# Kernel optimization log

Measured on AMD Instinct MI355X. Metric: run time of the kernel, lower is better.

## Reference

```python
import jax, jax.numpy as jnp
import numpy as np

B, S, D, H = 2, 2048, 1024, 16
DH = D // H  # head dim = 64


def _split_heads(x):
    # [B,S,D] -> [B,H,S,DH]
    return x.reshape(B, S, H, DH).transpose(0, 2, 1, 3)


def setup_inputs() -> dict:
    key = jax.random.key(0)
    ks = jax.random.split(key, 14)
    sc = 1.0 / np.sqrt(D)
    p = {"hidden_states": jax.random.normal(ks[0], (B, S, D), jnp.float32)}
    names = ["Wq", "Wk1", "Wk2", "Wv1", "Wv2", "Wd"]
    for i, n in enumerate(names):
        p[n] = jax.random.normal(ks[1 + 2 * i], (D, D), jnp.float32) * sc
        p["b" + n[1:]] = jax.random.normal(ks[2 + 2 * i], (D,), jnp.float32) * 0.02
    return p


def reference(hidden_states, Wq, bq, Wk1, bk1, Wk2, bk2, Wv1, bv1, Wv2, bv2, Wd, bd):
    q = _split_heads(hidden_states @ Wq + bq)
    k1 = _split_heads(hidden_states @ Wk1 + bk1)
    k2 = _split_heads(hidden_states @ Wk2 + bk2)
    v1 = _split_heads(hidden_states @ Wv1 + bv1)
    v2 = _split_heads(hidden_states @ Wv2 + bv2)

    scores = jnp.einsum("bhqd,bhkd->bhqk", q, k1) / np.sqrt(DH)
    causal = jnp.tril(jnp.ones((S, S), dtype=bool))  # True = keep
    scores = jnp.where(causal, scores, -jnp.inf)
    probs = jax.nn.softmax(scores, axis=-1)

    ctx = jnp.einsum("bhqk,bhkd->bhqd", probs, v1)          # [B,H,S,DH]
    ctx = jnp.einsum("bhqd,bhkd->bhqk", ctx, k2)            # [B,H,S,S]
    ctx = jnp.einsum("bhqk,bhkd->bhqd", ctx, v2)            # [B,H,S,DH]

    ctx = ctx.transpose(0, 2, 1, 3).reshape(B, S, D)
    return ctx @ Wd + bd
```

## Files before the change

### kernel.cpp

```cpp
#include <hip/hip_runtime.h>
#include <hip/hip_bf16.h>

typedef __bf16 bf16x8 __attribute__((ext_vector_type(8)));
typedef float f32x4 __attribute__((ext_vector_type(4)));
using bf16 = __hip_bfloat16;

#define SEQ 2048
#define DM 1024
#define NH 16
#define DH 64
#define NBH 32
#define MR 4096

#define WAITBAR(N) asm volatile("s_waitcnt vmcnt(" #N ")\n\ts_barrier" ::: "memory")

static __device__ __forceinline__ void async_cp16(const void* gsrc, void* ldsdst) {
  __builtin_amdgcn_global_load_lds((__attribute__((address_space(1))) void*)gsrc,
                                   (__attribute__((address_space(3))) void*)ldsdst, 16, 0, 0);
}

static __device__ __forceinline__ unsigned short f2bfu(float f) {
  bf16 h = __float2bfloat16(f);
  unsigned short u; __builtin_memcpy(&u, &h, 2); return u;
}
static __device__ __forceinline__ unsigned int pack_bf2(float lo, float hi) {
  return (unsigned int)f2bfu(lo) | ((unsigned int)f2bfu(hi) << 16);
}

__global__ __launch_bounds__(256) void cast_x(const float* __restrict__ X, bf16* __restrict__ Xb) {
  long g = ((long)blockIdx.x * 256 + threadIdx.x) * 8;
  float4 a = *(const float4*)(X + g);
  float4 b = *(const float4*)(X + g + 4);
  unsigned short u[8];
  u[0]=f2bfu(a.x); u[1]=f2bfu(a.y); u[2]=f2bfu(a.z); u[3]=f2bfu(a.w);
  u[4]=f2bfu(b.x); u[5]=f2bfu(b.y); u[6]=f2bfu(b.z); u[7]=f2bfu(b.w);
  uint4 o; __builtin_memcpy(&o, u, 16);
  *(uint4*)(Xb + g) = o;
}

struct WPtrs { const float* w[6]; };

__global__ __launch_bounds__(256) void transpose_cast_w(WPtrs wp, bf16* __restrict__ WtAll) {
  const int z = blockIdx.z;
  const float* W = wp.w[z];
  bf16* Wt = WtAll + (long)z * DM * DM;
  __shared__ float Ts[32][33];
  int n0 = blockIdx.x * 32, k0 = blockIdx.y * 32;
  int tx = threadIdx.x, ty = threadIdx.y;
#pragma unroll
  for (int it = 0; it < 4; ++it)
    Ts[ty + 8*it][tx] = W[(long)(k0 + ty + 8*it) * DM + n0 + tx];
  __syncthreads();
#pragma unroll
  for (int it = 0; it < 4; ++it)
    Wt[(long)(n0 + ty + 8*it) * DM + k0 + tx] = __float2bfloat16(Ts[tx][ty + 8*it]);
}

struct ProjArgs {
  const float* bias[5];
  bf16* out[5];
};

__global__ __launch_bounds__(256, 2) void gemm_proj(const bf16* __restrict__ A,
                                                    const bf16* __restrict__ WtAll, ProjArgs p) {
  __shared__ alignas(16) bf16 SM[36864];
  bf16* As = SM;
  bf16* Bs = SM + 12288;
  const int tid = threadIdx.x;
  const int bid = blockIdx.x;
  const int wave = tid >> 6, lane = tid & 63, l15 = lane & 15, l4 = lane >> 4;
  const int wm = wave >> 1, wn = wave & 1;
  const int slot8 = (l4 ^ ((l15 >> 1) & 3)) * 8;
  const int prow = tid >> 2;
  const int cc = (tid & 3) ^ ((prow >> 1) & 3);
  char* dA = (char*)As + wave * 1024;
  char* dB = (char*)Bs + wave * 1024;

  if (bid < 512) {
    const int mt = bid & 31, nt = bid >> 5;
    const int m0 = mt * 128;
    const int z = nt >> 2;
    const int n0z = (nt & 3) * 256;
    const bf16* Bt = WtAll + (long)z * DM * DM + (long)n0z * DM;

    const bf16* sA0 = A  + (long)(m0 + prow) * DM + cc * 8;
    const bf16* sA1 = sA0 + 64L * DM;
    const bf16* sB0 = Bt + (long)prow * DM + cc * 8;
    const bf16* sB1 = sB0 + 64L * DM;
    const bf16* sB2 = sB0 + 128L * DM;
    const bf16* sB3 = sB0 + 192L * DM;

#define PSTAGE(KT_, BUF_) do {                                  \
    int ko_ = (KT_) * 32;                                       \
    async_cp16(sA0 + ko_, dA + (BUF_) * 8192);                  \
    async_cp16(sA1 + ko_, dA + (BUF_) * 8192 + 4096);           \
    async_cp16(sB0 + ko_, dB + (BUF_) * 16384);                 \
    async_cp16(sB1 + ko_, dB + (BUF_) * 16384 + 4096);          \
    async_cp16(sB2 + ko_, dB + (BUF_) * 16384 + 8192);          \
    async_cp16(sB3 + ko_, dB + (BUF_) * 16384 + 12288);         \
  } while (0)

    const int arow = wm * 64 + l15;
    const int brow = wn * 128 + l15;
    f32x4 acc[4][8] = {};

#define PCOMPUTE(BUF_) do {                                                        \
    const bf16* ab_ = As + (BUF_) * 4096;                                          \
    const bf16* bb_ = Bs + (BUF_) * 8192;                                          \
    bf16x8 af_[4], bq_[8];                                                         \
    _Pragma("unroll")                                                              \
    for (int i = 0; i < 4; ++i) af_[i] = *(const bf16x8*)(ab_ + (arow + i * 16) * 32 + slot8); \
    _Pragma("unroll")                                                              \
    for (int j = 0; j < 8; ++j) bq_[j] = *(const bf16x8*)(bb_ + (brow + j * 16) * 32 + slot8); \
    _Pragma("unroll")                                                              \
    for (int i = 0; i < 4; ++i)                                                    \
      _Pragma("unroll")                                                            \
      for (int j = 0; j < 8; ++j)                                                  \
        acc[i][j] = __builtin_amdgcn_mfma_f32_16x16x32_bf16(af_[i], bq_[j], acc[i][j], 0, 0, 0); \
  } while (0)

    PSTAGE(0, 0);
    PSTAGE(1, 1);
    int buf = 0;
#pragma unroll 1
    for (int k = 0; k < 31; ++k) {
      WAITBAR(6);
      if (k < 30) {
        int nb = buf + 2; if (nb > 2) nb -= 3;
        PSTAGE(k + 2, nb);
      }
      PCOMPUTE(buf);
      ++buf; if (buf > 2) buf = 0;
    }
    WAITBAR(0);
    PCOMPUTE(buf);
#undef PSTAGE
#undef PCOMPUTE

    const float* bias = p.bias[z];
    bf16* out = p.out[z];
    float bv[8];
#pragma unroll
    for (int j = 0; j < 8; ++j) bv[j] = bias[n0z + wn * 128 + j * 16 + l15];

    if (z < 2) {
      const float scale = (z == 0) ? 0.125f * 1.44269504f : 1.0f;
#pragma unroll
      for (int i = 0; i < 4; ++i)
#pragma unroll
        for (int j = 0; j < 8; ++j)
#pragma unroll
          for (int r = 0; r < 4; ++r) {
            int m = m0 + wm * 64 + i * 16 + l4 * 4 + r;
            int n = n0z + wn * 128 + j * 16 + l15;
            int b = m >> 11, s = m & 2047, hh = n >> 6, d = n & 63;
            out[((long)((b * NH + hh) * SEQ + s)) * DH + d] =
                __float2bfloat16((acc[i][j][r] + bv[j]) * scale);
          }
    } else {
      __syncthreads();
      bf16* Os = SM;
#pragma unroll
      for (int i = 0; i < 4; ++i)
#pragma unroll
        for (int j = 0; j < 8; ++j)
#pragma unroll
          for (int r = 0; r < 4; ++r) {
            int nl = wn * 128 + j * 16 + l15;
            int ml = wm * 64 + i * 16 + l4 * 4 + r;
            Os[nl * 136 + ml] = __float2bfloat16(acc[i][j][r] + bv[j]);
          }
      __syncthreads();
      {
        int nl = tid;
        int ng = n0z + nl;
        int hh = ng >> 6, d = ng & 63;
        int b = m0 >> 11, s0 = m0 & 2047;
        bf16* op = out + ((long)((b * NH + hh) * DH + d)) * SEQ + s0;
#pragma unroll
        for (int u = 0; u < 16; ++u)
          *(bf16x8*)(op + u * 8) = *(const bf16x8*)(Os + nl * 136 + u * 8);
      }
    }
  } else {
    const int tb = bid - 512;
    const int mt = tb & 31, nt16 = tb >> 5;
    const int m0 = mt * 128, n0 = nt16 * 64;
    const bf16* Bt = WtAll + 4L * DM * DM + (long)n0 * DM;

    const bf16* sA0 = A + (long)(m0 + prow) * DM + cc * 8;
    const bf16* sA1 = sA0 + 64L * DM;
    const bf16* sB0 = Bt + (long)prow * DM + cc * 8;

#define TSTAGE(KT_, BUF_) do {                                  \
    int ko_ = (KT_) * 32;                                       \
    async_cp16(sA0 + ko_, dA + (BUF_) * 8192);                  \
    async_cp16(sA1 + ko_, dA + (BUF_) * 8192 + 4096);           \
    async_cp16(sB0 + ko_, dB + (BUF_) * 4096);                  \
  } while (0)

    const int arow = wm * 64 + l15;
    const int brow = wn * 32 + l15;
    f32x4 acc2[4][2] = {};

#define TCOMPUTE(BUF_) do {                                                        \
    const bf16* ab_ = As + (BUF_) * 4096;                                          \
    const bf16* bb_ = Bs + (BUF_) * 2048;                                          \
    bf16x8 af_[4], bq_[2];                                                         \
    _Pragma("unroll")                                                              \
    for (int i = 0; i < 4; ++i) af_[i] = *(const bf16x8*)(ab_ + (arow + i * 16) * 32 + slot8); \
    _Pragma("unroll")                                                              \
    for (int j = 0; j < 2; ++j) bq_[j] = *(const bf16x8*)(bb_ + (brow + j * 16) * 32 + slot8); \
    _Pragma("unroll")                                                              \
    for (int i = 0; i < 4; ++i)                                                    \
      _Pragma("unroll")                                                            \
      for (int j = 0; j < 2; ++j)                                                  \
        acc2[i][j] = __builtin_amdgcn_mfma_f32_16x16x32_bf16(af_[i], bq_[j], acc2[i][j], 0, 0, 0); \
  } while (0)

    TSTAGE(0, 0);
    TSTAGE(1, 1);
    int buf = 0;
#pragma unroll 1
    for (int k = 0; k < 31; ++k) {
      WAITBAR(3);
      if (k < 30) {
        int nb = buf + 2; if (nb > 2) nb -= 3;
        TSTAGE(k + 2, nb);
      }
      TCOMPUTE(buf);
      ++buf; if (buf > 2) buf = 0;
    }
    WAITBAR(0);
    TCOMPUTE(buf);
#undef TSTAGE
#undef TCOMPUTE

    float bv2[2];
#pragma unroll
    for (int j = 0; j < 2; ++j) bv2[j] = p.bias[4][n0 + wn * 32 + j * 16 + l15];
    __syncthreads();
    bf16* Os = SM;
#pragma unroll
    for (int i = 0; i < 4; ++i)
#pragma unroll
      for (int j = 0; j < 2; ++j)
#pragma unroll
        for (int r = 0; r < 4; ++r) {
          int nl = wn * 32 + j * 16 + l15;
          int ml = wm * 64 + i * 16 + l4 * 4 + r;
          Os[nl * 136 + ml] = __float2bfloat16(acc2[i][j][r] + bv2[j]);
        }
    __syncthreads();
    {
      int nl = tid & 63, seg = tid >> 6;
      int ng = n0 + nl;
      int hh = ng >> 6, d = ng & 63;
      int b = m0 >> 11, s0 = m0 & 2047;
      bf16* op = p.out[4] + ((long)((b * NH + hh) * DH + d)) * SEQ + s0 + seg * 32;
#pragma unroll
      for (int u = 0; u < 4; ++u)
        *(bf16x8*)(op + u * 8) = *(const bf16x8*)(Os + nl * 136 + seg * 32 + u * 8);
    }
  }
}

__global__ __launch_bounds__(256, 3) void gemm_out(const bf16* __restrict__ A, const bf16* __restrict__ Bt,
                                                   const float* __restrict__ bias, float* __restrict__ out) {
  __shared__ alignas(16) bf16 As[3 * 128 * 32];
  __shared__ alignas(16) bf16 Bs[3 * 64 * 32];
  const int tid = threadIdx.x;
  const int bid = blockIdx.x;
  const int nt = bid & 15, mt = bid >> 4;
  const int m0 = mt * 128, n0 = nt * 64;
  const int wave = tid >> 6, lane = tid & 63, l15 = lane & 15, l4 = lane >> 4;
  const int wm = wave >> 1, wn = wave & 1;
  const int slot8 = (l4 ^ ((l15 >> 1) & 3)) * 8;
  const int prow = tid >> 2;
  const int cc = (tid & 3) ^ ((prow >> 1) & 3);
  const bf16* sA0 = A + (long)(m0 + prow) * DM + cc * 8;
  const bf16* sA1 = sA0 + 64L * DM;
  const bf16* sB0 = Bt + (long)(n0 + prow) * DM + cc * 8;
  char* dA = (char*)As + wave * 1024;
  char* dB = (char*)Bs + wave * 1024;

#define OSTAGE(KT_, BUF_) do {                                  \
    int ko_ = (KT_) * 32;                                       \
    async_cp16(sA0 + ko_, dA + (BUF_) * 8192);                  \
    async_cp16(sA1 + ko_, dA + (BUF_) * 8192 + 4096);           \
    async_cp16(sB0 + ko_, dB + (BUF_) * 4096);                  \
  } while (0)

  const int arow = wm * 64 + l15;
  const int brow = wn * 32 + l15;
  f32x4 acc2[4][2] = {};

#define OCOMPUTE(BUF_) do {                                                        \
    const bf16* ab_ = As + (BUF_) * 4096;                                          \
    const bf16* bb_ = Bs + (BUF_) * 2048;                                          \
    bf16x8 af_[4], bq_[2];                                                         \
    _Pragma("unroll")                                                              \
    for (int i = 0; i < 4; ++i) af_[i] = *(const bf16x8*)(ab_ + (arow + i * 16) * 32 + slot8); \
    _Pragma("unroll")                                                              \
    for (int j = 0; j < 2; ++j) bq_[j] = *(const bf16x8*)(bb_ + (brow + j * 16) * 32 + slot8); \
    _Pragma("unroll")                                                              \
    for (int i = 0; i < 4; ++i)                                                    \
      _Pragma("unroll")                                                            \
      for (int j = 0; j < 2; ++j)                                                  \
        acc2[i][j] = __builtin_amdgcn_mfma_f32_16x16x32_bf16(af_[i], bq_[j], acc2[i][j], 0, 0, 0); \
  } while (0)

  OSTAGE(0, 0);
  OSTAGE(1, 1);
  int buf = 0;
#pragma unroll 1
  for (int k = 0; k < 31; ++k) {
    WAITBAR(3);
    if (k < 30) {
      int nb = buf + 2; if (nb > 2) nb -= 3;
      OSTAGE(k + 2, nb);
    }
    OCOMPUTE(buf);
    ++buf; if (buf > 2) buf = 0;
  }
  WAITBAR(0);
  OCOMPUTE(buf);
#undef OSTAGE
#undef OCOMPUTE

  float bv[2];
#pragma unroll
  for (int j = 0; j < 2; ++j) bv[j] = bias[n0 + wn * 32 + j * 16 + l15];
#pragma unroll
  for (int i = 0; i < 4; ++i)
#pragma unroll
    for (int j = 0; j < 2; ++j)
#pragma unroll
      for (int r = 0; r < 4; ++r) {
        int m = m0 + wm * 64 + i * 16 + l4 * 4 + r;
        int n = n0 + wn * 32 + j * 16 + l15;
        out[(long)m * DM + n] = acc2[i][j][r] + bv[j];
      }
}

__global__ __launch_bounds__(256) void m_kernel(
    const bf16* __restrict__ k2t, const bf16* __restrict__ v2t, float* __restrict__ Mbuf)
{
  const int scx = blockIdx.x;
  const int bh = blockIdx.y;
  const int tid = threadIdx.x, wave = tid >> 6, lane = tid & 63, l15 = lane & 15, l4 = lane >> 4;
  const bf16* kp = k2t + (long)bh * DH * SEQ;
  const bf16* vp = v2t + (long)bh * DH * SEQ;
  __shared__ alignas(16) bf16 K2s[64 * 32];
  __shared__ alignas(16) bf16 V2s[64 * 32];
  f32x4 acc[4] = {};
  const int s0 = scx * 256;
  for (int kk = 0; kk < 256; kk += 32) {
    __syncthreads();
    {
      int c = tid, r = c >> 2, pp = c & 3;
      async_cp16(kp + (long)r * SEQ + s0 + kk + pp * 8, K2s + wave * 64 * 8);
      async_cp16(vp + (long)r * SEQ + s0 + kk + pp * 8, V2s + wave * 64 * 8);
    }
    __syncthreads();
    int arow = 16 * wave + l15;
    bf16x8 a = *(const bf16x8*)(K2s + arow * 32 + l4 * 8);
#pragma unroll
    for (int nb = 0; nb < 4; ++nb) {
      int col = nb * 16 + l15;
      bf16x8 b = *(const bf16x8*)(V2s + col * 32 + l4 * 8);
      acc[nb] = __builtin_amdgcn_mfma_f32_16x16x32_bf16(a, b, acc[nb], 0, 0, 0);
    }
  }
  float* Mp = Mbuf + (long)bh * 4096;
#pragma unroll
  for (int nb = 0; nb < 4; ++nb)
#pragma unroll
    for (int r = 0; r < 4; ++r) {
      int row = 16 * wave + l4 * 4 + r;
      int col = nb * 16 + l15;
      atomicAdd(Mp + row * 64 + col, acc[nb][r]);
    }
}

static __device__ __forceinline__ void redist(const unsigned int (&pk)[4][2], bf16x8 (&pb)[2],
                                              int l4, int l15) {
#pragma unroll
  for (int h = 0; h < 2; ++h) {
    unsigned int w4[4];
#pragma unroll
    for (int w = 0; w < 4; ++w) {
      int src = l15 + 16 * (2 * (l4 & 1) + (w >> 1));
      unsigned int va = (unsigned int)__shfl((int)pk[2 * h][w & 1], src);
      unsigned int vb = (unsigned int)__shfl((int)pk[2 * h + 1][w & 1], src);
      w4[w] = (l4 & 2) ? vb : va;
    }
    __builtin_memcpy(&pb[h], w4, 16);
  }
}

__global__ __launch_bounds__(256) void attn_fused(
    const bf16* __restrict__ q,
    const bf16* __restrict__ k1,
    const bf16* __restrict__ v1t,
    const float* __restrict__ Mbuf,
    bf16* __restrict__ ctx2)
{
  const int bid = blockIdx.x;
  const int xcd = bid & 7, ii = bid >> 3;
  const int bh = (xcd << 2) | (ii & 3);
  const int qpair = ii >> 2;
  const int bb = bh >> 4, hh = bh & 15;
  const int tid = threadIdx.x, wave = tid >> 6, lane = tid & 63;
  const int l15 = lane & 15, l4 = lane >> 4;
  const bf16* qp = q   + (long)bh * SEQ * DH;
  const bf16* kp = k1  + (long)bh * SEQ * DH;
  const bf16* vp = v1t + (long)bh * DH * SEQ;
  const float* Mp = Mbuf + (long)bh * 4096;

  __shared__ alignas(16) bf16 Ks[2][128 * 64];
  __shared__ alignas(16) bf16 Vs[2][64 * 128];

  bf16x8 mf[4][2];
#pragma unroll
  for (int db = 0; db < 4; ++db)
#pragma unroll
    for (int h = 0; h < 2; ++h) {
      bf16x8 t;
#pragma unroll
      for (int j = 0; j < 8; ++j)
        t[j] = (__bf16)Mp[(32 * h + 8 * l4 + j) * 64 + 16 * db + l15];
      mf[db][h] = t;
    }

#define STAGE_KV(JJ, BUF) do {                                                     \
    int kv0_ = 128 * (JJ);                                                         \
    int cK_ = (tid & 7) ^ ((tid >> 3) & 7);                                        \
    int cV_ = (tid & 15) ^ ((tid >> 4) & 15);                                      \
    _Pragma("unroll")                                                              \
    for (int p_ = 0; p_ < 4; ++p_) {                                               \
      int rK_ = (tid >> 3) + 32 * p_;                                              \
      async_cp16(kp + (long)(kv0_ + rK_) * DH + cK_ * 8,                           \
                 (char*)Ks[BUF] + p_ * 4096 + wave * 1024);                        \
      int rV_ = (tid >> 4) + 16 * p_;                                              \
      async_cp16(vp + (long)rV_ * SEQ + kv0_ + cV_ * 8,                            \
                 (char*)Vs[BUF] + p_ * 4096 + wave * 1024);                        \
    }                                                                              \
  } while (0)

#pragma unroll 1
  for (int half = 0; half < 2; ++half) {
    const int tq = (half == 0) ? (31 - qpair) : qpair;
    const int Q0 = 64 * tq;
    const int qg = Q0 + 16 * wave + l15;
    const int jm = tq >> 1;

    __syncthreads();
    STAGE_KV(0, 0);

    bf16x8 aq[2];
#pragma unroll
    for (int h = 0; h < 2; ++h)
      aq[h] = *(const bf16x8*)(qp + (long)qg * DH + 32 * h + 8 * l4);

    float m_run = -__builtin_inff(), l_run = 0.f;
    f32x4 acc_o[4] = {};

    __syncthreads();

#pragma unroll 1
    for (int j = 0; j <= jm; ++j) {
      const int cur = j & 1;
      if (j < jm) STAGE_KV(j + 1, cur ^ 1);

      f32x4 sc[8] = {};
      __builtin_amdgcn_s_setprio(1);
#pragma unroll
      for (int nb = 0; nb < 8; ++nb) {
        const bf16* krow = Ks[cur] + (16 * nb + l15) * 64;
#pragma unroll
        for (int h = 0; h < 2; ++h) {
          bf16x8 kf = *(const bf16x8*)(krow + (((4 * h + l4) ^ (l15 & 7)) * 8));
          sc[nb] = __builtin_amdgcn_mfma_f32_16x16x32_bf16(kf, aq[h], sc[nb], 0, 0, 0);
        }
      }
      __builtin_amdgcn_s_setprio(0);

      if (j == jm) {
        const int kv0 = 128 * j;
#pragma unroll
        for (int nb = 0; nb < 8; ++nb)
#pragma unroll
          for (int r = 0; r < 4; ++r)
            if (kv0 + 16 * nb + 4 * l4 + r > qg) sc[nb][r] = -__builtin_inff();
      }

      float tmax = -__builtin_inff();
#pragma unroll
      for (int nb = 0; nb < 8; ++nb)
#pragma unroll
        for (int r = 0; r < 4; ++r) tmax = fmaxf(tmax, sc[nb][r]);
      tmax = fmaxf(tmax, __shfl_xor(tmax, 16));
      tmax = fmaxf(tmax, __shfl_xor(tmax, 32));

      if (!__all(tmax <= m_run)) {
        float mnew = fmaxf(m_run, tmax);
        float sf = __builtin_amdgcn_exp2f(m_run - mnew);
        m_run = mnew;
        l_run *= sf;
#pragma unroll
        for (int db = 0; db < 4; ++db)
#pragma unroll
          for (int r = 0; r < 4; ++r) acc_o[db][r] *= sf;
      }

      float ssum = 0.f;
      unsigned int pkA[4][2], pkB[4][2];
#pragma unroll
      for (int nb = 0; nb < 4; ++nb)
#pragma unroll
        for (int pr = 0; pr < 2; ++pr) {
          float p0 = __builtin_amdgcn_exp2f(sc[nb][2 * pr]     - m_run);
          float p1 = __builtin_amdgcn_exp2f(sc[nb][2 * pr + 1] - m_run);
          ssum += p0 + p1;
          pkA[nb][pr] = pack_bf2(p0, p1);
        }
#pragma unroll
      for (int nb = 0; nb < 4; ++nb)
#pragma unroll
        for (int pr = 0; pr < 2; ++pr) {
          float p0 = __builtin_amdgcn_exp2f(sc[nb + 4][2 * pr]     - m_run);
          float p1 = __builtin_amdgcn_exp2f(sc[nb + 4][2 * pr + 1] - m_run);
          ssum += p0 + p1;
          pkB[nb][pr] = pack_bf2(p0, p1);
        }
      ssum += __shfl_xor(ssum, 16);
      ssum += __shfl_xor(ssum, 32);
      l_run += ssum;

      bf16x8 pbA[2], pbB[2];
      redist(pkA, pbA, l4, l15);
      redist(pkB, pbB, l4, l15);
      __builtin_amdgcn_s_setprio(1);
#pragma unroll
      for (int db = 0; db < 4; ++db) {
        const bf16* vrow = Vs[cur] + (16 * db + l15) * 128;
#pragma unroll
        for (int hs = 0; hs < 2; ++hs) {
          bf16x8 vf = *(const bf16x8*)(vrow + (((4 * hs + l4) ^ l15) * 8));
          acc_o[db] = __builtin_amdgcn_mfma_f32_16x16x32_bf16(vf, pbA[hs], acc_o[db], 0, 0, 0);
        }
#pragma unroll
        for (int hs = 0; hs < 2; ++hs) {
          bf16x8 vf = *(const bf16x8*)(vrow + (((4 * (hs + 2) + l4) ^ l15) * 8));
          acc_o[db] = __builtin_amdgcn_mfma_f32_16x16x32_bf16(vf, pbB[hs], acc_o[db], 0, 0, 0);
        }
      }
      __builtin_amdgcn_s_setprio(0);
      __syncthreads();
    }

    float invl = __builtin_amdgcn_rcpf(l_run);
    unsigned int ck[4][2];
#pragma unroll
    for (int db = 0; db < 4; ++db)
#pragma unroll
      for (int pr = 0; pr < 2; ++pr)
        ck[db][pr] = pack_bf2(acc_o[db][2 * pr] * invl, acc_o[db][2 * pr + 1] * invl);
    bf16x8 cb[2];
    redist(ck, cb, l4, l15);
    f32x4 o2[4] = {};
#pragma unroll
    for (int db = 0; db < 4; ++db)
#pragma unroll
      for (int h = 0; h < 2; ++h)
        o2[db] = __builtin_amdgcn_mfma_f32_16x16x32_bf16(mf[db][h], cb[h], o2[db], 0, 0, 0);

    bf16* Os = (bf16*)Ks;
#pragma unroll
    for (int db = 0; db < 4; ++db)
#pragma unroll
      for (int r = 0; r < 4; ++r)
        Os[(16 * wave + l15) * 72 + 16 * db + 4 * l4 + r] = __float2bfloat16(o2[db][r]);
    __syncthreads();
    {
      int rr = tid >> 2, cc2 = tid & 3;
      long obase = ((long)(bb * SEQ + Q0 + rr)) * DM + hh * DH + cc2 * 16;
      *(bf16x8*)(ctx2 + obase)     = *(const bf16x8*)(Os + rr * 72 + cc2 * 16);
      *(bf16x8*)(ctx2 + obase + 8) = *(const bf16x8*)(Os + rr * 72 + cc2 * 16 + 8);
    }
  }
#undef STAGE_KV
}

extern "C" void kernel_launch(void* const* d_in, const int* in_sizes, int n_in,
                              void* d_out, int out_size, void* d_ws, size_t ws_size,
                              hipStream_t stream) {
  (void)in_sizes; (void)n_in; (void)out_size; (void)ws_size;
  const float* X = (const float*)d_in[0];
  const float* W[6]    = {(const float*)d_in[1], (const float*)d_in[3], (const float*)d_in[5],
                          (const float*)d_in[7], (const float*)d_in[9], (const float*)d_in[11]};
  const float* bias[6] = {(const float*)d_in[2], (const float*)d_in[4], (const float*)d_in[6],
                          (const float*)d_in[8], (const float*)d_in[10], (const float*)d_in[12]};

  char* ws = (char*)d_ws;
  bf16* Xb  = (bf16*)(ws);
  bf16* Wt  = (bf16*)(ws + (8L  << 20));
  bf16* qB  = (bf16*)(ws + (20L << 20));
  bf16* k1B = (bf16*)(ws + (28L << 20));
  bf16* k2t = (bf16*)(ws + (36L << 20));
  bf16* v1t = (bf16*)(ws + (44L << 20));
  bf16* v2t = (bf16*)(ws + (52L << 20));
  float* Mb = (float*)(ws + (60L << 20));
  bf16* c2  = Xb;

  cast_x<<<2048, 256, 0, stream>>>(X, Xb);

  WPtrs wp; for (int z = 0; z < 6; ++z) wp.w[z] = W[z];
  transpose_cast_w<<<dim3(32, 32, 6), dim3(32, 8), 0, stream>>>(wp, Wt);

  ProjArgs pa;
  for (int z = 0; z < 5; ++z) pa.bias[z] = bias[z];
  pa.out[0] = qB; pa.out[1] = k1B; pa.out[2] = k2t; pa.out[3] = v1t; pa.out[4] = v2t;
  gemm_proj<<<1024, 256, 0, stream>>>(Xb, Wt, pa);

  hipMemsetAsync(Mb, 0, (size_t)NBH * 4096 * 4, stream);
  m_kernel<<<dim3(8, 32), 256, 0, stream>>>(k2t, v2t, Mb);

  attn_fused<<<512, 256, 0, stream>>>(qB, k1B, v1t, Mb, c2);

  gemm_out<<<512, 256, 0, stream>>>(c2, Wt + 5L * DM * DM, bias[5], (float*)d_out);
}
```

Measured before the change: 146.4 us.

## Split attention waves 2x2 over query and key halves with LDS merge

Each wave now handles 32 query rows against half of each 128-key tile, not 16 query rows against the full tile. Every K and V fragment read from LDS feeds two MFMAs, which halves LDS fragment traffic per MFMA. The two key-half partial softmax states (m, l, acc) are merged through LDS at the end before the M projection. The cost is more accumulator registers, an extra merge pass with a barrier, and only half the waves doing the final projection.

```diff
diff --git a/kernel.cpp b/kernel.cpp
--- a/kernel.cpp
+++ b/kernel.cpp
@@ -413,6 +413,7 @@
   const int bb = bh >> 4, hh = bh & 15;
   const int tid = threadIdx.x, wave = tid >> 6, lane = tid & 63;
   const int l15 = lane & 15, l4 = lane >> 4;
+  const int wq = wave & 1, wk = wave >> 1;
   const bf16* qp = q   + (long)bh * SEQ * DH;
   const bf16* kp = k1  + (long)bh * SEQ * DH;
   const bf16* vp = v1t + (long)bh * DH * SEQ;
@@ -420,6 +421,8 @@
 
   __shared__ alignas(16) bf16 Ks[2][128 * 64];
   __shared__ alignas(16) bf16 Vs[2][64 * 128];
+  float* adF = (float*)Vs;
+  float* mlF = (float*)((char*)Ks + 16384);
 
   bf16x8 mf[4][2];
 #pragma unroll
@@ -452,19 +455,23 @@
   for (int half = 0; half < 2; ++half) {
     const int tq = (half == 0) ? (31 - qpair) : qpair;
     const int Q0 = 64 * tq;
-    const int qg = Q0 + 16 * wave + l15;
     const int jm = tq >> 1;
+    const int qg0 = Q0 + 32 * wq + l15;
+    const int qg1 = qg0 + 16;
 
     __syncthreads();
     STAGE_KV(0, 0);
 
-    bf16x8 aq[2];
-#pragma unroll
-    for (int h = 0; h < 2; ++h)
-      aq[h] = *(const bf16x8*)(qp + (long)qg * DH + 32 * h + 8 * l4);
-
-    float m_run = -__builtin_inff(), l_run = 0.f;
-    f32x4 acc_o[4] = {};
+    bf16x8 aq[2][2];
+#pragma unroll
+    for (int qt = 0; qt < 2; ++qt)
+#pragma unroll
+      for (int h = 0; h < 2; ++h)
+        aq[qt][h] = *(const bf16x8*)(qp + (long)(qg0 + 16 * qt) * DH + 32 * h + 8 * l4);
+
+    float m_run[2] = {-__builtin_inff(), -__builtin_inff()};
+    float l_run[2] = {0.f, 0.f};
+    f32x4 acc_o[4][2] = {};
 
     __syncthreads();
 
@@ -473,117 +480,159 @@
       const int cur = j & 1;
       if (j < jm) STAGE_KV(j + 1, cur ^ 1);
 
-      f32x4 sc[8] = {};
+      f32x4 sc[4][2] = {};
       __builtin_amdgcn_s_setprio(1);
 #pragma unroll
-      for (int nb = 0; nb < 8; ++nb) {
-        const bf16* krow = Ks[cur] + (16 * nb + l15) * 64;
+      for (int nb = 0; nb < 4; ++nb) {
+        const bf16* krow = Ks[cur] + (64 * wk + 16 * nb + l15) * 64;
 #pragma unroll
         for (int h = 0; h < 2; ++h) {
           bf16x8 kf = *(const bf16x8*)(krow + (((4 * h + l4) ^ (l15 & 7)) * 8));
-          sc[nb] = __builtin_amdgcn_mfma_f32_16x16x32_bf16(kf, aq[h], sc[nb], 0, 0, 0);
+          sc[nb][0] = __builtin_amdgcn_mfma_f32_16x16x32_bf16(kf, aq[0][h], sc[nb][0], 0, 0, 0);
+          sc[nb][1] = __builtin_amdgcn_mfma_f32_16x16x32_bf16(kf, aq[1][h], sc[nb][1], 0, 0, 0);
         }
       }
       __builtin_amdgcn_s_setprio(0);
 
       if (j == jm) {
-        const int kv0 = 128 * j;
-#pragma unroll
-        for (int nb = 0; nb < 8; ++nb)
-#pragma unroll
-          for (int r = 0; r < 4; ++r)
-            if (kv0 + 16 * nb + 4 * l4 + r > qg) sc[nb][r] = -__builtin_inff();
-      }
-
-      float tmax = -__builtin_inff();
-#pragma unroll
-      for (int nb = 0; nb < 8; ++nb)
-#pragma unroll
-        for (int r = 0; r < 4; ++r) tmax = fmaxf(tmax, sc[nb][r]);
-      tmax = fmaxf(tmax, __shfl_xor(tmax, 16));
-      tmax = fmaxf(tmax, __shfl_xor(tmax, 32));
-
-      if (!__all(tmax <= m_run)) {
-        float mnew = fmaxf(m_run, tmax);
-        float sf = __builtin_amdgcn_exp2f(m_run - mnew);
-        m_run = mnew;
-        l_run *= sf;
-#pragma unroll
-        for (int db = 0; db < 4; ++db)
-#pragma unroll
-          for (int r = 0; r < 4; ++r) acc_o[db][r] *= sf;
-      }
-
-      float ssum = 0.f;
-      unsigned int pkA[4][2], pkB[4][2];
-#pragma unroll
-      for (int nb = 0; nb < 4; ++nb)
-#pragma unroll
-        for (int pr = 0; pr < 2; ++pr) {
-          float p0 = __builtin_amdgcn_exp2f(sc[nb][2 * pr]     - m_run);
-          float p1 = __builtin_amdgcn_exp2f(sc[nb][2 * pr + 1] - m_run);
-          ssum += p0 + p1;
-          pkA[nb][pr] = pack_bf2(p0, p1);
+        const int kv0 = 128 * j + 64 * wk;
+#pragma unroll
+        for (int nb = 0; nb < 4; ++nb)
+#pragma unroll
+          for (int r = 0; r < 4; ++r) {
+            int kvg = kv0 + 16 * nb + 4 * l4 + r;
+            if (kvg > qg0) sc[nb][0][r] = -__builtin_inff();
+            if (kvg > qg1) sc[nb][1][r] = -__builtin_inff();
+          }
+      }
+
+      float tmax[2];
+#pragma unroll
+      for (int qt = 0; qt < 2; ++qt) {
+        float v = -__builtin_inff();
+#pragma unroll
+        for (int nb = 0; nb < 4; ++nb)
+#pragma unroll
+          for (int r = 0; r < 4; ++r) v = fmaxf(v, sc[nb][qt][r]);
+        v = fmaxf(v, __shfl_xor(v, 16));
+        v = fmaxf(v, __shfl_xor(v, 32));
+        tmax[qt] = v;
+      }
+
+      if (!__all((tmax[0] <= m_run[0]) & (tmax[1] <= m_run[1]))) {
+#pragma unroll
+        for (int qt = 0; qt < 2; ++qt) {
+          float mnew = fmaxf(m_run[qt], tmax[qt]);
+          float sf = __builtin_amdgcn_exp2f(m_run[qt] - mnew);
+          m_run[qt] = mnew;
+          l_run[qt] *= sf;
+#pragma unroll
+          for (int db = 0; db < 4; ++db)
+#pragma unroll
+            for (int r = 0; r < 4; ++r) acc_o[db][qt][r] *= sf;
         }
-#pragma unroll
-      for (int nb = 0; nb < 4; ++nb)
-#pragma unroll
-        for (int pr = 0; pr < 2; ++pr) {
-          float p0 = __builtin_amdgcn_exp2f(sc[nb + 4][2 * pr]     - m_run);
-          float p1 = __builtin_amdgcn_exp2f(sc[nb + 4][2 * pr + 1] - m_run);
-          ssum += p0 + p1;
-          pkB[nb][pr] = pack_bf2(p0, p1);
-        }
-      ssum += __shfl_xor(ssum, 16);
-      ssum += __shfl_xor(ssum, 32);
-      l_run += ssum;
-
-      bf16x8 pbA[2], pbB[2];
-      redist(pkA, pbA, l4, l15);
-      redist(pkB, pbB, l4, l15);
+      }
+
+      unsigned int pk[2][4][2];
+#pragma unroll
+      for (int qt = 0; qt < 2; ++qt) {
+        float msub = (m_run[qt] < -1e37f) ? 0.f : m_run[qt];
+        float ssum = 0.f;
+#pragma unroll
+        for (int nb = 0; nb < 4; ++nb)
+#pragma unroll
+          for (int pr = 0; pr < 2; ++pr) {
+            float p0 = __builtin_amdgcn_exp2f(sc[nb][qt][2 * pr]     - msub);
+            float p1 = __builtin_amdgcn_exp2f(sc[nb][qt][2 * pr + 1] - msub);
+            ssum += p0 + p1;
+            pk[qt][nb][pr] = pack_bf2(p0, p1);
+          }
+        ssum += __shfl_xor(ssum, 16);
+        ssum += __shfl_xor(ssum, 32);
+        l_run[qt] += ssum;
+      }
+
+      bf16x8 pb[2][2];
+      redist(pk[0], pb[0], l4, l15);
+      redist(pk[1], pb[1], l4, l15);
       __builtin_amdgcn_s_setprio(1);
 #pragma unroll
       for (int db = 0; db < 4; ++db) {
         const bf16* vrow = Vs[cur] + (16 * db + l15) * 128;
 #pragma unroll
         for (int hs = 0; hs < 2; ++hs) {
-          bf16x8 vf = *(const bf16x8*)(vrow + (((4 * hs + l4) ^ l15) * 8));
-          acc_o[db] = __builtin_amdgcn_mfma_f32_16x16x32_bf16(vf, pbA[hs], acc_o[db], 0, 0, 0);
-        }
-#pragma unroll
-        for (int hs = 0; hs < 2; ++hs) {
-          bf16x8 vf = *(const bf16x8*)(vrow + (((4 * (hs + 2) + l4) ^ l15) * 8));
-          acc_o[db] = __builtin_amdgcn_mfma_f32_16x16x32_bf16(vf, pbB[hs], acc_o[db], 0, 0, 0);
+          bf16x8 vf = *(const bf16x8*)(vrow + (((8 * wk + 4 * hs + l4) ^ l15) * 8));
+          acc_o[db][0] = __builtin_amdgcn_mfma_f32_16x16x32_bf16(vf, pb[0][hs], acc_o[db][0], 0, 0, 0);
+          acc_o[db][1] = __builtin_amdgcn_mfma_f32_16x16x32_bf16(vf, pb[1][hs], acc_o[db][1], 0, 0, 0);
         }
       }
       __builtin_amdgcn_s_setprio(0);
       __syncthreads();
     }
 
-    float invl = __builtin_amdgcn_rcpf(l_run);
-    unsigned int ck[4][2];
 #pragma unroll
     for (int db = 0; db < 4; ++db)
 #pragma unroll
-      for (int pr = 0; pr < 2; ++pr)
-        ck[db][pr] = pack_bf2(acc_o[db][2 * pr] * invl, acc_o[db][2 * pr + 1] * invl);
-    bf16x8 cb[2];
-    redist(ck, cb, l4, l15);
-    f32x4 o2[4] = {};
-#pragma unroll
-    for (int db = 0; db < 4; ++db)
-#pragma unroll
-      for (int h = 0; h < 2; ++h)
-        o2[db] = __builtin_amdgcn_mfma_f32_16x16x32_bf16(mf[db][h], cb[h], o2[db], 0, 0, 0);
-
-    bf16* Os = (bf16*)Ks;
-#pragma unroll
-    for (int db = 0; db < 4; ++db)
-#pragma unroll
-      for (int r = 0; r < 4; ++r)
-        Os[(16 * wave + l15) * 72 + 16 * db + 4 * l4 + r] = __float2bfloat16(o2[db][r]);
+      for (int qt = 0; qt < 2; ++qt)
+#pragma unroll
+        for (int r = 0; r < 4; ++r)
+          adF[wave * 2048 + lane * 32 + db * 8 + qt * 4 + r] = acc_o[db][qt][r];
+#pragma unroll
+    for (int qt = 0; qt < 2; ++qt) {
+      mlF[wave * 64 + qt * 16 + l15] = m_run[qt];
+      mlF[wave * 64 + 32 + qt * 16 + l15] = l_run[qt];
+    }
+    __syncthreads();
+
+    if (wk == 0) {
+      const int w2 = wave + 2;
+      float aS[2], bS[2], invl[2];
+#pragma unroll
+      for (int qt = 0; qt < 2; ++qt) {
+        float mB = mlF[w2 * 64 + qt * 16 + l15];
+        float lB = mlF[w2 * 64 + 32 + qt * 16 + l15];
+        float ms = fmaxf(m_run[qt], mB);
+        aS[qt] = __builtin_amdgcn_exp2f(m_run[qt] - ms);
+        bS[qt] = __builtin_amdgcn_exp2f(mB - ms);
+        invl[qt] = __builtin_amdgcn_rcpf(l_run[qt] * aS[qt] + lB * bS[qt]);
+      }
+      unsigned int ck[2][4][2];
+#pragma unroll
+      for (int qt = 0; qt < 2; ++qt)
+#pragma unroll
+        for (int db = 0; db < 4; ++db)
+#pragma unroll
+          for (int pr = 0; pr < 2; ++pr) {
+            float g0 = (acc_o[db][qt][2 * pr]     * aS[qt] +
+                        adF[w2 * 2048 + lane * 32 + db * 8 + qt * 4 + 2 * pr]     * bS[qt]) * invl[qt];
+            float g1 = (acc_o[db][qt][2 * pr + 1] * aS[qt] +
+                        adF[w2 * 2048 + lane * 32 + db * 8 + qt * 4 + 2 * pr + 1] * bS[qt]) * invl[qt];
+            ck[qt][db][pr] = pack_bf2(g0, g1);
+          }
+      bf16x8 cb[2][2];
+      redist(ck[0], cb[0], l4, l15);
+      redist(ck[1], cb[1], l4, l15);
+      f32x4 o2[4][2] = {};
+#pragma unroll
+      for (int db = 0; db < 4; ++db)
+#pragma unroll
+        for (int qt = 0; qt < 2; ++qt)
+#pragma unroll
+          for (int h = 0; h < 2; ++h)
+            o2[db][qt] = __builtin_amdgcn_mfma_f32_16x16x32_bf16(mf[db][h], cb[qt][h], o2[db][qt], 0, 0, 0);
+
+      bf16* Os = (bf16*)Ks;
+#pragma unroll
+      for (int db = 0; db < 4; ++db)
+#pragma unroll
+        for (int qt = 0; qt < 2; ++qt)
+#pragma unroll
+          for (int r = 0; r < 4; ++r)
+            Os[(32 * wq + 16 * qt + l15) * 72 + 16 * db + 4 * l4 + r] = __float2bfloat16(o2[db][qt][r]);
+    }
     __syncthreads();
     {
+      const bf16* Os = (const bf16*)Ks;
       int rr = tid >> 2, cc2 = tid & 3;
       long obase = ((long)(bb * SEQ + Q0 + rr)) * DM + hh * DH + cc2 * 16;
       *(bf16x8*)(ctx2 + obase)     = *(const bf16x8*)(Os + rr * 72 + cc2 * 16);
```

New measurement: 154.1 us. 1.05x slower.
